# Optimization experiments

Hardware: AMD Instinct MI355X
Metric: run time of the kernel (lower is better)

## Reference

```python
import jax, jax.numpy as jnp
import numpy as np

VOCAB, EMB, UNITS, OUT = 10000, 256, 128, 2
B, T = 256, 1024


def setup_inputs() -> dict:
    key = jax.random.key(0)
    ks = jax.random.split(key, 7)
    x = jax.random.randint(ks[0], (B, T), 0, VOCAB, dtype=jnp.int32)
    emb_table = jax.random.normal(ks[1], (VOCAB, EMB), dtype=jnp.float32) * 0.05
    # Keras LSTM: kernel [EMB,4U], recurrent_kernel [U,4U], bias [4U]; gate order i,f,c,o
    Wk = jax.random.normal(ks[2], (EMB, 4 * UNITS), dtype=jnp.float32) * 0.05
    Wr = jax.random.normal(ks[3], (UNITS, 4 * UNITS), dtype=jnp.float32) * 0.05
    b = jax.random.normal(ks[4], (4 * UNITS,), dtype=jnp.float32) * 0.05
    Wd = jax.random.normal(ks[5], (UNITS, OUT), dtype=jnp.float32) * 0.05
    bd = jax.random.normal(ks[6], (OUT,), dtype=jnp.float32) * 0.05
    return {"x": x, "emb_table": emb_table, "Wk": Wk, "Wr": Wr, "b": b, "Wd": Wd, "bd": bd}


def _lstm_relu(e, Wk, Wr, b):
    # e: [B, T, EMB]. activation='relu' (cell/out), recurrent_activation=sigmoid.
    xg = jnp.einsum('bte,eg->btg', e, Wk) + b          # precompute input gates [B,T,4U]
    xg = jnp.transpose(xg, (1, 0, 2))                   # [T, B, 4U]

    def step(carry, xg_t):
        h, c = carry
        z = xg_t + h @ Wr                               # [B, 4U]
        zi, zf, zc, zo = jnp.split(z, 4, axis=-1)       # Keras gate order i,f,c,o
        i = jax.nn.sigmoid(zi)
        f = jax.nn.sigmoid(zf)
        g = jax.nn.relu(zc)
        o = jax.nn.sigmoid(zo)
        c_new = f * c + i * g
        h_new = o * jax.nn.relu(c_new)
        return (h_new, c_new), None

    batch = e.shape[0]
    h0 = jnp.zeros((batch, Wr.shape[0]), dtype=e.dtype)
    c0 = jnp.zeros((batch, Wr.shape[0]), dtype=e.dtype)
    (h_last, _), _ = jax.lax.scan(step, (h0, c0), xg)
    return h_last                                       # [B, U] (return_sequences=False)


def reference(x, emb_table, Wk, Wr, b, Wd, bd):
    e = emb_table[x]                                    # [B, T, EMB] embedding lookup
    h = _lstm_relu(e, Wk, Wr, b)                        # [B, U]
    return h @ Wd + bd                                  # [B, 2]
```

## Files before the change

kernel.cpp:

```cpp
#include <hip/hip_runtime.h>

typedef __bf16 bf16_t;
typedef __attribute__((ext_vector_type(8))) __bf16 bf16x8;
typedef __attribute__((ext_vector_type(4))) float f32x4;
typedef unsigned short u16;
typedef unsigned int u32;
typedef unsigned long long u64;

#define TC 128
#define NCH 8
#define XGHALF 16777216
#define LDA 264
#define LOG2E 1.44269504f

#define LDS_BARRIER() asm volatile("s_waitcnt lgkmcnt(0)\n\ts_barrier" ::: "memory")

#if __has_builtin(__builtin_amdgcn_exp2f)
#define EXP2F __builtin_amdgcn_exp2f
#else
static __device__ __forceinline__ float EXP2F(float x) {
  float r;
  asm volatile("v_exp_f32 %0, %1\n\ts_nop 1" : "=v"(r) : "v"(x));
  return r;
}
#endif


static __device__ __forceinline__ u16 bf16bits(float v) {
  return __builtin_bit_cast(u16, (bf16_t)v);
}
static __device__ __forceinline__ float bf16f(u16 v) {
  return __builtin_bit_cast(float, (u32)v << 16);
}

__global__ __launch_bounds__(512) void k_fused(
    const int* __restrict__ x, const float* __restrict__ emb,
    u16* __restrict__ embb, const float* __restrict__ Wk,
    u16* __restrict__ wkt, const float* __restrict__ Wr,
    u16* __restrict__ wrt, const float* __restrict__ bias,
    const float* __restrict__ Wd, const float* __restrict__ bd,
    u16* __restrict__ xg, float* __restrict__ hstf, float* __restrict__ cstf,
    float* __restrict__ out, int cs) {
  const int tid = threadIdx.x;
  const int w = tid >> 6, lane = tid & 63;
  const int l16 = lane & 15, quad = lane >> 4;

  if (blockIdx.x >= 585) {
    for (int i = (blockIdx.x - 585) * 512 + tid; i < 2560000; i += 262144)
      embb[i] = bf16bits(emb[i]);
    return;
  }
  if (blockIdx.x == 584) {
    const int u = 16 * w + l16;
#pragma unroll
    for (int j = 0; j < 4; ++j) {
      const float sj = (j == 2) ? 1.0f : -LOG2E;
#pragma unroll
      for (int kt = 0; kt < 4; ++kt)
#pragma unroll
        for (int jj = 0; jj < 8; ++jj)
          wrt[tid * 128 + (j * 4 + kt) * 8 + jj] =
              bf16bits(Wr[(kt * 32 + quad * 8 + jj) * 512 + u + 128 * j] * sj);
    }
    return;
  }
  if (blockIdx.x >= 576) {
    for (int i = (blockIdx.x - 576) * 512 + tid; i < 131072; i += 4096) {
      int k = i & 255, n = i >> 8;
      wkt[i] = bf16bits(Wk[k * 512 + n]);
    }
    return;
  }

  if (blockIdx.x >= 64) {
    const int cb = cs + 1;
    if (cb >= NCH) return;
    const bool raw = (cs < 0);
    const int tau = blockIdx.x - 64;
    const int gg = tau >> 5, tb = tau & 31;
    u16* xgc = xg + (size_t)(cb & 1) * XGHALF;
    __shared__ u16 Al[64 * LDA];
    __shared__ float biasl[512];

    bf16x8 bfr[4][8];
    if (raw) {
#pragma unroll
      for (int nt = 0; nt < 4; ++nt)
#pragma unroll
        for (int kt = 0; kt < 8; ++kt)
#pragma unroll
          for (int jj = 0; jj < 8; ++jj)
            bfr[nt][kt][jj] =
                (bf16_t)Wk[(kt * 32 + quad * 8 + jj) * 512 + 64 * w + 16 * nt + l16];
    } else {
#pragma unroll
      for (int nt = 0; nt < 4; ++nt) {
        const u16* bp = wkt + (64 * w + 16 * nt + l16) * 256 + quad * 8;
#pragma unroll
        for (int kt = 0; kt < 8; ++kt)
          bfr[nt][kt] = *(const bf16x8*)(bp + kt * 32);
      }
    }

#pragma unroll
    for (int p = 0; p < 4; ++p) {
      int f = p * 512 + tid;
      int lr = f >> 5, ch = f & 31;
      int xi = (16 * gg + (lr & 15)) * 1024 + cb * TC + tb * 4 + (lr >> 4);
      int idx = x[xi];
      if (raw) {
        const float* ep = emb + idx * 256 + ch * 8;
        u16 tmp[8];
#pragma unroll
        for (int e = 0; e < 8; ++e) tmp[e] = bf16bits(ep[e]);
        *(uint4*)&Al[lr * LDA + ch * 8] = *(const uint4*)tmp;
      } else {
        *(uint4*)&Al[lr * LDA + ch * 8] = *(const uint4*)&embb[idx * 256 + ch * 8];
      }
    }
    biasl[tid] = bias[tid];
    __syncthreads();

    f32x4 acc[4][4];
#pragma unroll
    for (int mt = 0; mt < 4; ++mt)
#pragma unroll
      for (int nt = 0; nt < 4; ++nt) acc[mt][nt] = f32x4{0.f, 0.f, 0.f, 0.f};
#pragma unroll
    for (int kt = 0; kt < 8; ++kt) {
      bf16x8 a[4];
#pragma unroll
      for (int mt = 0; mt < 4; ++mt)
        a[mt] = *(const bf16x8*)&Al[(mt * 16 + l16) * LDA + kt * 32 + quad * 8];
#pragma unroll
      for (int nt = 0; nt < 4; ++nt)
#pragma unroll
        for (int mt = 0; mt < 4; ++mt)
          acc[mt][nt] = __builtin_amdgcn_mfma_f32_16x16x32_bf16(
              a[mt], bfr[nt][kt], acc[mt][nt], 0, 0, 0);
    }

    const float gsc = ((w >> 1) == 2) ? 1.0f : -LOG2E;
    const size_t gtbase = ((size_t)(4 * gg + quad) * TC + tb * 4) * 2048;
#pragma unroll
    for (int nt = 0; nt < 4; ++nt) {
      float bv = biasl[64 * w + 16 * nt + l16];
      int tile = 4 * w + nt;
#pragma unroll
      for (int mt = 0; mt < 4; ++mt) {
        u64 pk = 0;
#pragma unroll
        for (int r = 0; r < 4; ++r)
          pk |= (u64)bf16bits((acc[mt][nt][r] + bv) * gsc) << (16 * r);
        size_t off = gtbase + (size_t)mt * 2048 + tile * 64 + l16 * 4;
        *(u64*)&xgc[off] = pk;
      }
    }
  } else {
    if (cs < 0) return;
    const int g = blockIdx.x;
    const int u = 16 * w + l16;
    __shared__ __align__(16) u16 hbuf[2][4 * 144];
    __shared__ __align__(16) u16 zrow[128];

    bf16x8 wf[4][4];
    {
      const u16* wp = wrt + tid * 128;
#pragma unroll
      for (int j = 0; j < 4; ++j)
#pragma unroll
        for (int kt = 0; kt < 4; ++kt)
          wf[j][kt] = *(const bf16x8*)(wp + (j * 4 + kt) * 8);
    }
    if (tid < 128) zrow[tid] = 0;

    float c1 = 0.f, h1 = 0.f;
    if (cs != 0) {
      c1 = cstf[(g * 4 + quad) * 128 + u];
      h1 = hstf[(g * 4 + quad) * 128 + u];
    }
    hbuf[0][quad * 144 + u] = bf16bits(h1);

    const bool ald = (l16 & 3) == 0;
    const u16* rd0 = ald ? &hbuf[0][(l16 >> 2) * 144 + quad * 8] : &zrow[quad * 8];
    const u16* rd1 = ald ? &hbuf[1][(l16 >> 2) * 144 + quad * 8] : &zrow[quad * 8];
    u16* wr0 = &hbuf[0][quad * 144 + u];
    u16* wr1 = &hbuf[1][quad * 144 + u];

    const u16* xp = xg + (size_t)(cs & 1) * XGHALF + (size_t)g * TC * 2048 +
                    w * 64 + l16 * 4 + quad;
    u16 xq0[4], xq1[4];
#pragma unroll
    for (int j = 0; j < 4; ++j) xq0[j] = xp[j * 512];
#pragma unroll
    for (int j = 0; j < 4; ++j) xq1[j] = xp[2048 + j * 512];
    xp += 2 * 2048;

    __syncthreads();

    auto halfstep = [&](const u16* rd, u16* wr, u16* xv) {
      bf16x8 a[4];
#pragma unroll
      for (int kt = 0; kt < 4; ++kt)
        a[kt] = *(const bf16x8*)(rd + kt * 32);
      f32x4 acc[4];
#pragma unroll
      for (int j = 0; j < 4; ++j)
        acc[j] = f32x4{bf16f(xv[j]), 0.f, 0.f, 0.f};
#pragma unroll
      for (int j = 0; j < 4; ++j)
#pragma unroll
        for (int kt = 0; kt < 4; ++kt)
          acc[j] = __builtin_amdgcn_mfma_f32_16x16x32_bf16(a[kt], wf[j][kt],
                                                           acc[j], 0, 0, 0);
#pragma unroll
      for (int j = 0; j < 4; ++j) xv[j] = xp[j * 512];
      xp += 2048;
      float ig = __builtin_amdgcn_rcpf(1.f + EXP2F(acc[0][0]));
      float fg = __builtin_amdgcn_rcpf(1.f + EXP2F(acc[1][0]));
      float og = __builtin_amdgcn_rcpf(1.f + EXP2F(acc[3][0]));
      float gg = fmaxf(acc[2][0], 0.f);
      c1 = fg * c1 + ig * gg;
      h1 = og * fmaxf(c1, 0.f);
      *wr = bf16bits(h1);
      LDS_BARRIER();
    };

    for (int t2 = 0; t2 < TC; t2 += 2) {
      halfstep(rd0, wr1, xq0);
      halfstep(rd1, wr0, xq1);
    }

    if (cs != NCH - 1) {
      cstf[(g * 4 + quad) * 128 + u] = c1;
      hstf[(g * 4 + quad) * 128 + u] = h1;
    } else if (tid < 8) {
      int p = tid >> 1, jo = tid & 1;
      float o = bd[jo];
      for (int k = 0; k < 128; ++k)
        o += bf16f(hbuf[0][p * 144 + k]) * Wd[k * 2 + jo];
      out[(g * 4 + p) * 2 + jo] = o;
    }
  }
}

extern "C" void kernel_launch(void* const* d_in, const int* in_sizes, int n_in,
                              void* d_out, int out_size, void* d_ws, size_t ws_size,
                              hipStream_t stream) {
  const int* x = (const int*)d_in[0];
  const float* emb = (const float*)d_in[1];
  const float* Wk = (const float*)d_in[2];
  const float* Wr = (const float*)d_in[3];
  const float* bias = (const float*)d_in[4];
  const float* Wd = (const float*)d_in[5];
  const float* bd = (const float*)d_in[6];
  float* out = (float*)d_out;
  char* ws = (char*)d_ws;
  u16* xg = (u16*)(ws);
  u16* embb = (u16*)(ws + 67108864);
  u16* wkt = (u16*)(ws + 72228864);
  float* hst = (float*)(ws + 72491008);
  float* cst = (float*)(ws + 72622080);
  u16* wrt = (u16*)(ws + 72753152);

  for (int cs = -1; cs < NCH; ++cs) {
    int nwg = (cs < 0) ? 1097 : ((cs + 1 < NCH) ? 576 : 64);
    k_fused<<<nwg, 512, 0, stream>>>(x, emb, embb, Wk, wkt, Wr, wrt, bias,
                                     Wd, bd, xg, hst, cst, out, cs);
  }
}
```

Measured before the change: 604.8 us.

## Split weight prep into its own launch and shorten recurrent MFMA dependency chain

The bf16 conversion of the embedding table and weights moves into a separate preliminary launch, so the first input-gate chunk reads the converted tables instead of taking a slower fp32 'raw' path. In the recurrent step, the accumulator now starts from zero and the precomputed input-gate term is added after the MFMAs. This takes the xg load off the start of the matrix chain. The MFMAs are also interleaved across gates so consecutive ones are independent. The zero-padding LDS row is dropped in favour of duplicated h rows, and the recurrent waves get raised scheduling priority. The cost is one extra kernel launch before the chunk loop.

After: 606.6 us. Within noise of the previous version (+0.3%).

```diff
diff --git a/kernel.cpp b/kernel.cpp
--- a/kernel.cpp
+++ b/kernel.cpp
@@ -45,29 +45,28 @@
   const int w = tid >> 6, lane = tid & 63;
   const int l16 = lane & 15, quad = lane >> 4;
 
-  if (blockIdx.x >= 585) {
-    for (int i = (blockIdx.x - 585) * 512 + tid; i < 2560000; i += 262144)
-      embb[i] = bf16bits(emb[i]);
-    return;
-  }
-  if (blockIdx.x == 584) {
-    const int u = 16 * w + l16;
-#pragma unroll
-    for (int j = 0; j < 4; ++j) {
-      const float sj = (j == 2) ? 1.0f : -LOG2E;
-#pragma unroll
-      for (int kt = 0; kt < 4; ++kt)
-#pragma unroll
-        for (int jj = 0; jj < 8; ++jj)
-          wrt[tid * 128 + (j * 4 + kt) * 8 + jj] =
-              bf16bits(Wr[(kt * 32 + quad * 8 + jj) * 512 + u + 128 * j] * sj);
-    }
-    return;
-  }
-  if (blockIdx.x >= 576) {
-    for (int i = (blockIdx.x - 576) * 512 + tid; i < 131072; i += 4096) {
-      int k = i & 255, n = i >> 8;
-      wkt[i] = bf16bits(Wk[k * 512 + n]);
+  if (cs == -2) {
+    const int bid = blockIdx.x;
+    if (bid >= 9) {
+      for (int i = (bid - 9) * 512 + tid; i < 2560000; i += 262144)
+        embb[i] = bf16bits(emb[i]);
+    } else if (bid == 8) {
+      const int u = 16 * w + l16;
+#pragma unroll
+      for (int j = 0; j < 4; ++j) {
+        const float sj = (j == 2) ? 1.0f : -LOG2E;
+#pragma unroll
+        for (int kt = 0; kt < 4; ++kt)
+#pragma unroll
+          for (int jj = 0; jj < 8; ++jj)
+            wrt[tid * 128 + (j * 4 + kt) * 8 + jj] =
+                bf16bits(Wr[(kt * 32 + quad * 8 + jj) * 512 + u + 128 * j] * sj);
+      }
+    } else {
+      for (int i = bid * 512 + tid; i < 131072; i += 4096) {
+        int k = i & 255, n = i >> 8;
+        wkt[i] = bf16bits(Wk[k * 512 + n]);
+      }
     }
     return;
   }
@@ -75,7 +74,6 @@
   if (blockIdx.x >= 64) {
     const int cb = cs + 1;
     if (cb >= NCH) return;
-    const bool raw = (cs < 0);
     const int tau = blockIdx.x - 64;
     const int gg = tau >> 5, tb = tau & 31;
     u16* xgc = xg + (size_t)(cb & 1) * XGHALF;
@@ -83,23 +81,12 @@
     __shared__ float biasl[512];
 
     bf16x8 bfr[4][8];
-    if (raw) {
-#pragma unroll
-      for (int nt = 0; nt < 4; ++nt)
-#pragma unroll
-        for (int kt = 0; kt < 8; ++kt)
-#pragma unroll
-          for (int jj = 0; jj < 8; ++jj)
-            bfr[nt][kt][jj] =
-                (bf16_t)Wk[(kt * 32 + quad * 8 + jj) * 512 + 64 * w + 16 * nt + l16];
-    } else {
-#pragma unroll
-      for (int nt = 0; nt < 4; ++nt) {
-        const u16* bp = wkt + (64 * w + 16 * nt + l16) * 256 + quad * 8;
-#pragma unroll
-        for (int kt = 0; kt < 8; ++kt)
-          bfr[nt][kt] = *(const bf16x8*)(bp + kt * 32);
-      }
+#pragma unroll
+    for (int nt = 0; nt < 4; ++nt) {
+      const u16* bp = wkt + (64 * w + 16 * nt + l16) * 256 + quad * 8;
+#pragma unroll
+      for (int kt = 0; kt < 8; ++kt)
+        bfr[nt][kt] = *(const bf16x8*)(bp + kt * 32);
     }
 
 #pragma unroll
@@ -108,15 +95,7 @@
       int lr = f >> 5, ch = f & 31;
       int xi = (16 * gg + (lr & 15)) * 1024 + cb * TC + tb * 4 + (lr >> 4);
       int idx = x[xi];
-      if (raw) {
-        const float* ep = emb + idx * 256 + ch * 8;
-        u16 tmp[8];
-#pragma unroll
-        for (int e = 0; e < 8; ++e) tmp[e] = bf16bits(ep[e]);
-        *(uint4*)&Al[lr * LDA + ch * 8] = *(const uint4*)tmp;
-      } else {
-        *(uint4*)&Al[lr * LDA + ch * 8] = *(const uint4*)&embb[idx * 256 + ch * 8];
-      }
+      *(uint4*)&Al[lr * LDA + ch * 8] = *(const uint4*)&embb[idx * 256 + ch * 8];
     }
     biasl[tid] = bias[tid];
     __syncthreads();
@@ -161,7 +140,8 @@
     const int g = blockIdx.x;
     const int u = 16 * w + l16;
     __shared__ __align__(16) u16 hbuf[2][4 * 144];
-    __shared__ __align__(16) u16 zrow[128];
+
+    __builtin_amdgcn_s_setprio(1);
 
     bf16x8 wf[4][4];
     {
@@ -172,7 +152,6 @@
         for (int kt = 0; kt < 4; ++kt)
           wf[j][kt] = *(const bf16x8*)(wp + (j * 4 + kt) * 8);
     }
-    if (tid < 128) zrow[tid] = 0;
 
     float c1 = 0.f, h1 = 0.f;
     if (cs != 0) {
@@ -181,9 +160,8 @@
     }
     hbuf[0][quad * 144 + u] = bf16bits(h1);
 
-    const bool ald = (l16 & 3) == 0;
-    const u16* rd0 = ald ? &hbuf[0][(l16 >> 2) * 144 + quad * 8] : &zrow[quad * 8];
-    const u16* rd1 = ald ? &hbuf[1][(l16 >> 2) * 144 + quad * 8] : &zrow[quad * 8];
+    const u16* rd0 = &hbuf[0][(l16 >> 2) * 144 + quad * 8];
+    const u16* rd1 = &hbuf[1][(l16 >> 2) * 144 + quad * 8];
     u16* wr0 = &hbuf[0][quad * 144 + u];
     u16* wr1 = &hbuf[1][quad * 144 + u];
 
@@ -203,23 +181,29 @@
 #pragma unroll
       for (int kt = 0; kt < 4; ++kt)
         a[kt] = *(const bf16x8*)(rd + kt * 32);
+      const f32x4 c0 = {0.f, 0.f, 0.f, 0.f};
       f32x4 acc[4];
 #pragma unroll
       for (int j = 0; j < 4; ++j)
-        acc[j] = f32x4{bf16f(xv[j]), 0.f, 0.f, 0.f};
-#pragma unroll
-      for (int j = 0; j < 4; ++j)
-#pragma unroll
-        for (int kt = 0; kt < 4; ++kt)
+        acc[j] =
+            __builtin_amdgcn_mfma_f32_16x16x32_bf16(a[0], wf[j][0], c0, 0, 0, 0);
+#pragma unroll
+      for (int kt = 1; kt < 4; ++kt)
+#pragma unroll
+        for (int j = 0; j < 4; ++j)
           acc[j] = __builtin_amdgcn_mfma_f32_16x16x32_bf16(a[kt], wf[j][kt],
                                                            acc[j], 0, 0, 0);
+      float zi = acc[0][0] + bf16f(xv[0]);
+      float zf = acc[1][0] + bf16f(xv[1]);
+      float zc = acc[2][0] + bf16f(xv[2]);
+      float zo = acc[3][0] + bf16f(xv[3]);
 #pragma unroll
       for (int j = 0; j < 4; ++j) xv[j] = xp[j * 512];
       xp += 2048;
-      float ig = __builtin_amdgcn_rcpf(1.f + EXP2F(acc[0][0]));
-      float fg = __builtin_amdgcn_rcpf(1.f + EXP2F(acc[1][0]));
-      float og = __builtin_amdgcn_rcpf(1.f + EXP2F(acc[3][0]));
-      float gg = fmaxf(acc[2][0], 0.f);
+      float ig = __builtin_amdgcn_rcpf(1.f + EXP2F(zi));
+      float fg = __builtin_amdgcn_rcpf(1.f + EXP2F(zf));
+      float og = __builtin_amdgcn_rcpf(1.f + EXP2F(zo));
+      float gg = fmaxf(zc, 0.f);
       c1 = fg * c1 + ig * gg;
       h1 = og * fmaxf(c1, 0.f);
       *wr = bf16bits(h1);
@@ -263,8 +247,10 @@
   float* cst = (float*)(ws + 72622080);
   u16* wrt = (u16*)(ws + 72753152);
 
+  k_fused<<<521, 512, 0, stream>>>(x, emb, embb, Wk, wkt, Wr, wrt, bias, Wd,
+                                   bd, xg, hst, cst, out, -2);
   for (int cs = -1; cs < NCH; ++cs) {
-    int nwg = (cs < 0) ? 1097 : ((cs + 1 < NCH) ? 576 : 64);
+    int nwg = (cs + 1 < NCH) ? 576 : 64;
     k_fused<<<nwg, 512, 0, stream>>>(x, emb, embb, Wk, wkt, Wr, wrt, bias,
                                      Wd, bd, xg, hst, cst, out, cs);
   }
```
